# Optimization experiments

Measured on AMD Instinct MI355X. Metric: run time of the kernel, lower is better.

The kernel has to match this reference:

```python
import jax, jax.numpy as jnp
import numpy as np

S, B, T = 16, 32, 64        # max_sents, batch, max_tokens
V, E, H = 50000, 256, 256   # vocab, embed_size, gru_hidden (n_dim)
NC = 50                     # n_classes


def setup_inputs() -> dict:
    key = jax.random.key(0)
    ks = jax.random.split(key, 30)

    def u(k, shape, s=0.1):
        return jax.random.uniform(k, shape, minval=-s, maxval=s, dtype=jnp.float32)

    return {
        "x": jax.random.randint(ks[0], (S, B, T), 0, V, dtype=jnp.int64),
        "embed": jax.random.normal(ks[1], (V, E), dtype=jnp.float32) * 0.1,
        # word-level bi-GRU (input E, hidden H); gate order r,z,n as in torch
        "wg_Wih_f": u(ks[2], (3 * H, E)), "wg_Whh_f": u(ks[3], (3 * H, H)),
        "wg_bih_f": u(ks[4], (3 * H,)),   "wg_bhh_f": u(ks[5], (3 * H,)),
        "wg_Wih_b": u(ks[6], (3 * H, E)), "wg_Whh_b": u(ks[7], (3 * H, H)),
        "wg_bih_b": u(ks[8], (3 * H,)),   "wg_bhh_b": u(ks[9], (3 * H,)),
        "word_W": u(ks[10], (2 * H, 2 * H)),
        "word_b": u(ks[11], (2 * H, 1)),
        "word_proj": u(ks[12], (2 * H, 1)),
        # sentence-level bi-GRU (input 2H, hidden H)
        "sg_Wih_f": u(ks[13], (3 * H, 2 * H)), "sg_Whh_f": u(ks[14], (3 * H, H)),
        "sg_bih_f": u(ks[15], (3 * H,)),       "sg_bhh_f": u(ks[16], (3 * H,)),
        "sg_Wih_b": u(ks[17], (3 * H, 2 * H)), "sg_Whh_b": u(ks[18], (3 * H, H)),
        "sg_bih_b": u(ks[19], (3 * H,)),       "sg_bhh_b": u(ks[20], (3 * H,)),
        "sent_W": u(ks[21], (2 * H, 2 * H)),
        "sent_b": u(ks[22], (2 * H, 1)),
        "sent_proj": u(ks[23], (2 * H, 1)),
        "fin_W": u(ks[24], (NC, 2 * H)),
        "fin_b": u(ks[25], (NC,)),
        "state_word": jnp.zeros((2, B, H), dtype=jnp.float32),
        "state_sent": jnp.zeros((2, B, H), dtype=jnp.float32),
    }


def _gru_dir(x, h0, Wih, Whh, bih, bhh, reverse=False):
    # x: [T, B, in]; returns hidden states [T, B, H] (in original time order)
    xp = jnp.einsum('tbe,ge->tbg', x, Wih) + bih  # precompute input projections

    def step(h, xt):
        g = h @ Whh.T + bhh
        xr, xz, xn = jnp.split(xt, 3, axis=-1)
        hr, hz, hn = jnp.split(g, 3, axis=-1)
        r = jax.nn.sigmoid(xr + hr)
        z = jax.nn.sigmoid(xz + hz)
        n = jnp.tanh(xn + r * hn)
        h = (1.0 - z) * n + z * h
        return h, h

    _, hs = jax.lax.scan(step, h0, xp, reverse=reverse)
    return hs


def _bigru(x, h0, Wf, Hf, bif, bhf, Wb, Hb, bib, bhb):
    f = _gru_dir(x, h0[0], Wf, Hf, bif, bhf, reverse=False)
    b = _gru_dir(x, h0[1], Wb, Hb, bib, bhb, reverse=True)
    return jnp.concatenate([f, b], axis=-1)  # [T, B, 2H]


def _attn_pool(out, W, b, proj):
    # out: [T, B, 2H]; batch_matmul_bias(tanh) -> batch_matmul -> softmax over T -> weighted sum
    squish = jnp.tanh(jnp.einsum('tbh,hk->tbk', out, W) + b[:, 0])  # [T,B,2H]
    scores = jnp.einsum('tbk,k->tb', squish, proj[:, 0])            # [T,B]
    a = jax.nn.softmax(scores, axis=0)                              # softmax over seq
    return jnp.einsum('tb,tbh->bh', a, out)                         # [B,2H]


def reference(x, embed,
              wg_Wih_f, wg_Whh_f, wg_bih_f, wg_bhh_f,
              wg_Wih_b, wg_Whh_b, wg_bih_b, wg_bhh_b,
              word_W, word_b, word_proj,
              sg_Wih_f, sg_Whh_f, sg_bih_f, sg_bhh_f,
              sg_Wih_b, sg_Whh_b, sg_bih_b, sg_bhh_b,
              sent_W, sent_b, sent_proj,
              fin_W, fin_b, state_word, state_sent):
    e = embed[x]                         # [S,B,T,E]
    e = jnp.transpose(e, (0, 2, 1, 3))   # [S,T,B,E] (torch code transposes per sentence)

    word_out = jax.vmap(
        lambda xs: _bigru(xs, state_word,
                          wg_Wih_f, wg_Whh_f, wg_bih_f, wg_bhh_f,
                          wg_Wih_b, wg_Whh_b, wg_bih_b, wg_bhh_b)
    )(e)                                 # [S,T,B,2H]

    s = jax.vmap(lambda o: _attn_pool(o, word_W, word_b, word_proj))(word_out)  # [S,B,2H]

    sent_out = _bigru(s, state_sent,
                      sg_Wih_f, sg_Whh_f, sg_bih_f, sg_bhh_f,
                      sg_Wih_b, sg_Whh_b, sg_bih_b, sg_bhh_b)  # [S,B,2H]
    pooled = _attn_pool(sent_out, sent_W, sent_b, sent_proj)   # [B,2H]
    return pooled @ fin_W.T + fin_b                            # [B,NC] logits
```

## Files before the change

### kernel.cpp

```cpp
#include <hip/hip_runtime.h>


typedef float  f32x4  __attribute__((ext_vector_type(4)));
typedef int    i32x4  __attribute__((ext_vector_type(4)));
typedef __bf16 bf16x8 __attribute__((ext_vector_type(8)));

#define DEVINL static __device__ __forceinline__

DEVINL unsigned short f2bf(float f) {
    unsigned int x = __builtin_bit_cast(unsigned int, f);
    x = x + 0x7fffu + ((x >> 16) & 1u);
    return (unsigned short)(x >> 16);
}
DEVINL float bf2f(unsigned short u) {
    unsigned int x = ((unsigned int)u) << 16;
    return __builtin_bit_cast(float, x);
}
DEVINL float sigm(float x) { return __builtin_amdgcn_rcpf(1.f + __expf(-x)); }
DEVINL float tanh_(float x) {
    x = fminf(fmaxf(x, -20.f), 20.f);
    float e = __expf(-2.f * x);
    return (1.f - e) * __builtin_amdgcn_rcpf(1.f + e);
}
DEVINL void mfma16(f32x4& acc, i32x4 a, i32x4 b) {
    acc = __builtin_amdgcn_mfma_f32_16x16x32_bf16(
        __builtin_bit_cast(bf16x8, a), __builtin_bit_cast(bf16x8, b), acc, 0, 0, 0);
}
DEVINL f32x4 zero4() { f32x4 v = {0.f, 0.f, 0.f, 0.f}; return v; }
DEVINL void gload16(const void* gsrc, void* ldst) {
    __builtin_amdgcn_global_load_lds(
        (const __attribute__((address_space(1))) unsigned int*)gsrc,
        (__attribute__((address_space(3))) unsigned int*)ldst, 16, 0, 0);
}

#define O_WPWF    ((size_t)0)
#define O_WPWB    ((size_t)1048576)
#define O_WPSGIH  ((size_t)2097152)
#define O_WPSHHF  ((size_t)3670016)
#define O_WPSHHB  ((size_t)4063232)
#define O_WPWW    ((size_t)4456448)
#define O_WPSW    ((size_t)4980736)
#define O_BIASWF  ((size_t)5505024)
#define O_BIASWB  ((size_t)5509120)
#define O_BIHCAT  ((size_t)5513216)
#define O_WOUT    ((size_t)5519360)
#define O_SCORESW ((size_t)39073792)
#define O_SSFRAG  ((size_t)39204864)
#define O_XPSENT  ((size_t)39729152)
#define O_SOFRAG  ((size_t)42874880)
#define O_SCORESS ((size_t)43399168)
#define WS_NEED_B ((size_t)43401216)
#define O_EMB16   ((size_t)43401216)
#define O_XPW     ((size_t)69001216)
#define WS_NEED_A ((size_t)169664512)

__global__ void k_prep(const float* wihf, const float* whhf,
                       const float* wihb, const float* whhb,
                       const float* sgihf, const float* sgihb,
                       const float* sghhf, const float* sghhb,
                       const float* wordW, const float* sentW,
                       const float* bihf, const float* bhhf,
                       const float* bihb, const float* bhhb,
                       const float* sgbihf, const float* sgbihb,
                       const float* sgbhhf, const float* sgbhhb,
                       const float* embed,
                       unsigned short* Wpwf, unsigned short* Wpwb,
                       unsigned short* Wpsgih,
                       unsigned short* WpshhF, unsigned short* WpshhB,
                       unsigned short* WpwW, unsigned short* WpsW,
                       float* biasWf, float* biasWb, float* bihCat,
                       unsigned short* emb16, int doEmb)
{
    const int tid0 = blockIdx.x * blockDim.x + threadIdx.x;
    const int nth  = gridDim.x * blockDim.x;

    for (int idx = tid0; idx < 2 * 524288; idx += nth) {
        int d = idx >> 19, sidx = idx & 524287;
        int j = sidx & 7, chunk = sidx >> 3;
        int lane = chunk & 63, nk = chunk >> 6;
        int kf = nk & 15, nf = nk >> 4;
        int n = nf * 16 + (lane & 15);
        int k = kf * 32 + (lane >> 4) * 8 + j;
        const float* Wih = d ? wihb : wihf;
        const float* Whh = d ? whhb : whhf;
        int g4 = n >> 8, jj = n & 255;
        float v = 0.f;
        if (k < 256) {
            if (g4 == 0) v = Wih[jj * 256 + k];
            else if (g4 == 1) v = Wih[(256 + jj) * 256 + k];
            else if (g4 == 2) v = Wih[(512 + jj) * 256 + k];
        } else {
            int kk = k - 256;
            if (g4 == 0) v = Whh[jj * 256 + kk];
            else if (g4 == 1) v = Whh[(256 + jj) * 256 + kk];
            else if (g4 == 3) v = Whh[(512 + jj) * 256 + kk];
        }
        (d ? Wpwb : Wpwf)[sidx] = f2bf(v);
    }
    for (int idx = tid0; idx < 786432; idx += nth) {
        int j = idx & 7, chunk = idx >> 3;
        int lane = chunk & 63, nk = chunk >> 6;
        int kf = nk & 15, nf = nk >> 4;
        int n = nf * 16 + (lane & 15);
        int k = kf * 32 + (lane >> 4) * 8 + j;
        float v = (n < 768) ? sgihf[n * 512 + k] : sgihb[(n - 768) * 512 + k];
        Wpsgih[idx] = f2bf(v);
    }
    for (int idx = tid0; idx < 2 * 196608; idx += nth) {
        int d = idx >= 196608;
        int sidx = d ? idx - 196608 : idx;
        int j = sidx & 7, chunk = sidx >> 3;
        int lane = chunk & 63, nk = chunk >> 6;
        int kf = nk & 7, nf = nk >> 3;
        int n = nf * 16 + (lane & 15);
        int k = kf * 32 + (lane >> 4) * 8 + j;
        float v = (d ? sghhb : sghhf)[n * 256 + k];
        (d ? WpshhB : WpshhF)[sidx] = f2bf(v);
    }
    for (int idx = tid0; idx < 2 * 262144; idx += nth) {
        int d = idx >> 18, sidx = idx & 262143;
        int j = sidx & 7, chunk = sidx >> 3;
        int lane = chunk & 63, nk = chunk >> 6;
        int kf = nk & 15, nf = nk >> 4;
        int n = nf * 16 + (lane & 15);
        int k = kf * 32 + (lane >> 4) * 8 + j;
        float v = (d ? sentW : wordW)[k * 512 + n];
        (d ? WpsW : WpwW)[sidx] = f2bf(v);
    }
    for (int idx = tid0; idx < 2048; idx += nth) {
        int d = idx >> 10, i = idx & 1023;
        int g4 = i >> 8, j = i & 255;
        const float* bi = d ? bihb : bihf;
        const float* bh = d ? bhhb : bhhf;
        float v = (g4 == 0) ? bi[j] + bh[j]
                : (g4 == 1) ? bi[256 + j] + bh[256 + j]
                : (g4 == 2) ? bi[512 + j] : bh[512 + j];
        (d ? biasWb : biasWf)[i] = v;
    }
    for (int idx = tid0; idx < 1536; idx += nth) {
        int d = idx >= 768, j = d ? idx - 768 : idx;
        const float* bi = d ? sgbihb : sgbihf;
        const float* bh = d ? sgbhhb : sgbhhf;
        bihCat[idx] = bi[j] + ((j < 512) ? bh[j] : 0.f);
    }
    if (doEmb) {
        for (int idx = tid0; idx < 3200000; idx += nth) {
            f32x4 v = ((const f32x4*)embed)[idx];
            unsigned int lo = (unsigned)f2bf(v.x) | ((unsigned)f2bf(v.y) << 16);
            unsigned int hi = (unsigned)f2bf(v.z) | ((unsigned)f2bf(v.w) << 16);
            ((unsigned int*)emb16)[idx * 2]     = lo;
            ((unsigned int*)emb16)[idx * 2 + 1] = hi;
        }
    }
}

__global__ __launch_bounds__(512)
void k_xpw(const int* xg, const unsigned short* emb16,
           const unsigned short* Wpwf_u, const unsigned short* Wpwb_u,
           const float* biasWf, const float* biasWb, unsigned short* xpw)
{
    __shared__ unsigned short Abuf[128][256];
    const int tid = threadIdx.x, lane = tid & 63, w = tid >> 6;
    const int cid = blockIdx.x;
    const int tq = cid & 3, bh = (cid >> 2) & 1, dir = (cid >> 3) & 1, s = cid >> 4;
    const int t0 = tq * 16;
    const i32x4* Wp = (const i32x4*)(dir ? Wpwb_u : Wpwf_u);
    const float* biasW = dir ? biasWb : biasWf;

    i32x4 B[3][2][8];
#pragma unroll
    for (int g = 0; g < 3; ++g)
#pragma unroll
        for (int q = 0; q < 2; ++q)
#pragma unroll
            for (int kk = 0; kk < 8; ++kk)
                B[g][q][kk] = Wp[((g * 16 + w * 2 + q) * 16 + kk) * 64 + lane];

    float bias_rg[3][2];
#pragma unroll
    for (int g = 0; g < 3; ++g)
#pragma unroll
        for (int q = 0; q < 2; ++q)
            bias_rg[g][q] = biasW[g * 256 + (w * 2 + q) * 16 + (lane & 15)];

    for (int ch = 0; ch < 2; ++ch) {
        __syncthreads();
#pragma unroll
        for (int c = 0; c < 8; ++c) {
            const int trow = 16 * w + 2 * c + (lane >> 5);
            const int b = trow & 15;
            const int tok = xg[(s * 32 + bh * 16 + b) * 64 + (t0 + ch * 8 + w)];
            const int kbyte = ((lane & 31) * 16) ^ ((trow & 7) << 4);
            gload16((const char*)emb16 + (size_t)tok * 512 + kbyte,
                    (char*)&Abuf[0][0] + (w * 8 + c) * 1024);
        }
        __syncthreads();

#pragma unroll 1
        for (int tl = 0; tl < 8; ++tl) {
            f32x4 acc[3][2];
#pragma unroll
            for (int g = 0; g < 3; ++g) { acc[g][0] = zero4(); acc[g][1] = zero4(); }
#pragma unroll
            for (int kk = 0; kk < 8; ++kk) {
                const int row = tl * 16 + (lane & 15);
                const int boff = (kk * 64 + (lane >> 4) * 16) ^ ((row & 7) << 4);
                i32x4 a = *(const i32x4*)((const char*)&Abuf[row][0] + boff);
#pragma unroll
                for (int g = 0; g < 3; ++g) {
                    mfma16(acc[g][0], a, B[g][0][kk]);
                    mfma16(acc[g][1], a, B[g][1][kk]);
                }
            }
            const int t = t0 + ch * 8 + tl;
            const int tb = (((s * 2 + dir) * 2 + bh) * 64 + t) * 12288;
#pragma unroll
            for (int g = 0; g < 3; ++g)
#pragma unroll
                for (int q = 0; q < 2; ++q) {
                    const int j = (w * 2 + q) * 16 + (lane & 15);
                    const float bb = bias_rg[g][q];
                    unsigned int lo = (unsigned)f2bf(acc[g][q][0] + bb) |
                                      ((unsigned)f2bf(acc[g][q][1] + bb) << 16);
                    unsigned int hi = (unsigned)f2bf(acc[g][q][2] + bb) |
                                      ((unsigned)f2bf(acc[g][q][3] + bb) << 16);
                    uint2 pk; pk.x = lo; pk.y = hi;
                    *(uint2*)(xpw + tb + (g * 256 + j) * 16 + 4 * (lane >> 4)) = pk;
                }
        }
    }
}

__global__ __launch_bounds__(512)
void k_gru_wordA(const float* stateW,
                 const unsigned short* Wpwf_u, const unsigned short* Wpwb_u,
                 const float* biasWf, const float* biasWb,
                 const unsigned short* xpw, unsigned short* wout)
{
    __shared__ unsigned short Abuf[2][16][256];
    __shared__ unsigned short xpL[2][12288];
    const int tid = threadIdx.x, lane = tid & 63, w = tid >> 6;
    const int cid = blockIdx.x;
    const int bh = cid & 1, dir = (cid >> 1) & 1, s = cid >> 2;
    const i32x4* Wp = (const i32x4*)(dir ? Wpwb_u : Wpwf_u);
    const float* biasW = dir ? biasWb : biasWf;
    const int gmap[3] = {0, 1, 3};

    i32x4 B[3][2][8];
#pragma unroll
    for (int g = 0; g < 3; ++g)
#pragma unroll
        for (int q = 0; q < 2; ++q)
#pragma unroll
            for (int kk = 0; kk < 8; ++kk)
                B[g][q][kk] = Wp[((gmap[g] * 16 + w * 2 + q) * 16 + 8 + kk) * 64 + lane];

    float bhn[2];
    float hreg[2][4];
#pragma unroll
    for (int q = 0; q < 2; ++q) {
        const int j = (w * 2 + q) * 16 + (lane & 15);
        bhn[q] = biasW[768 + j];
#pragma unroll
        for (int i = 0; i < 4; ++i) {
            const int b = 4 * (lane >> 4) + i;
            float h0 = stateW[dir * 8192 + (bh * 16 + b) * 256 + j];
            hreg[q][i] = h0;
            int byteoff = b * 512 + ((j * 2) ^ ((b & 7) << 4));
            *(unsigned short*)((char*)&Abuf[0][0][0] + byteoff) = f2bf(h0);
        }
    }
    const size_t xbase = (size_t)(((s * 2 + dir) * 2 + bh) * 64) * 24576;
    const int tfirst = dir ? 63 : 0;
#pragma unroll
    for (int c = 0; c < 3; ++c)
        gload16((const char*)xpw + xbase + (size_t)tfirst * 24576 +
                    ((w * 3 + c) * 64 + lane) * 16,
                (char*)&xpL[0][0] + (w * 3 + c) * 1024);

    for (int ti = 0; ti < 64; ++ti) {
        __syncthreads();
        const int t = dir ? 63 - ti : ti;
        const int cur = ti & 1, nxt = cur ^ 1;
        if (ti < 63) {
            const int tn = dir ? t - 1 : t + 1;
#pragma unroll
            for (int c = 0; c < 3; ++c)
                gload16((const char*)xpw + xbase + (size_t)tn * 24576 +
                            ((w * 3 + c) * 64 + lane) * 16,
                        (char*)&xpL[nxt][0] + (w * 3 + c) * 1024);
        }
        f32x4 acc[3][2];
#pragma unroll
        for (int g = 0; g < 3; ++g) { acc[g][0] = zero4(); acc[g][1] = zero4(); }
#pragma unroll
        for (int kk = 0; kk < 8; ++kk) {
            const int row = lane & 15;
            const int boff = (kk * 64 + (lane >> 4) * 16) ^ ((row & 7) << 4);
            i32x4 a = *(const i32x4*)((const char*)&Abuf[cur][row][0] + boff);
#pragma unroll
            for (int g = 0; g < 3; ++g) {
                mfma16(acc[g][0], a, B[g][0][kk]);
                mfma16(acc[g][1], a, B[g][1][kk]);
            }
        }
#pragma unroll
        for (int q = 0; q < 2; ++q) {
            const int j = (w * 2 + q) * 16 + (lane & 15);
            uint2 xr = *(const uint2*)((const char*)&xpL[cur][0] +
                        ((0 * 256 + j) * 16 + 4 * (lane >> 4)) * 2);
            uint2 xz = *(const uint2*)((const char*)&xpL[cur][0] +
                        ((1 * 256 + j) * 16 + 4 * (lane >> 4)) * 2);
            uint2 xn = *(const uint2*)((const char*)&xpL[cur][0] +
                        ((2 * 256 + j) * 16 + 4 * (lane >> 4)) * 2);
            float xrf[4] = { bf2f((unsigned short)(xr.x & 0xffffu)),
                             bf2f((unsigned short)(xr.x >> 16)),
                             bf2f((unsigned short)(xr.y & 0xffffu)),
                             bf2f((unsigned short)(xr.y >> 16)) };
            float xzf[4] = { bf2f((unsigned short)(xz.x & 0xffffu)),
                             bf2f((unsigned short)(xz.x >> 16)),
                             bf2f((unsigned short)(xz.y & 0xffffu)),
                             bf2f((unsigned short)(xz.y >> 16)) };
            float xnf[4] = { bf2f((unsigned short)(xn.x & 0xffffu)),
                             bf2f((unsigned short)(xn.x >> 16)),
                             bf2f((unsigned short)(xn.y & 0xffffu)),
                             bf2f((unsigned short)(xn.y >> 16)) };
#pragma unroll
            for (int i = 0; i < 4; ++i) {
                const int b = 4 * (lane >> 4) + i;
                float rv = sigm(xrf[i] + acc[0][q][i]);
                float zv = sigm(xzf[i] + acc[1][q][i]);
                float nv = tanh_(xnf[i] + rv * (acc[2][q][i] + bhn[q]));
                float hnew = (1.f - zv) * nv + zv * hreg[q][i];
                hreg[q][i] = hnew;
                unsigned short hb = f2bf(hnew);
                int byteoff = b * 512 + ((j * 2) ^ ((b & 7) << 4));
                *(unsigned short*)((char*)&Abuf[nxt][0][0] + byteoff) = hb;
                const int r = (s * 64 + t) * 32 + bh * 16 + b;
                const int hcol = dir * 256 + j;
                wout[(((r >> 4) * 16 + (hcol >> 5)) * 64 + (r & 15) +
                      ((hcol >> 3) & 3) * 16) * 8 + (hcol & 7)] = hb;
            }
        }
    }
}

DEVINL void prefetchE(unsigned short (*Ab)[512], const int* xg, const float* embed,
                      int s, int t, int tid)
{
    const int brow = tid >> 5, c = tid & 31;
    const int tok = xg[(s * 32 + brow) * 64 + t];
    const f32x4* src = (const f32x4*)(embed + (size_t)tok * 256) + c * 2;
    f32x4 f0 = src[0], f1 = src[1];
    i32x4 pk;
    pk.x = (int)((unsigned)f2bf(f0.x) | ((unsigned)f2bf(f0.y) << 16));
    pk.y = (int)((unsigned)f2bf(f0.z) | ((unsigned)f2bf(f0.w) << 16));
    pk.z = (int)((unsigned)f2bf(f1.x) | ((unsigned)f2bf(f1.y) << 16));
    pk.w = (int)((unsigned)f2bf(f1.z) | ((unsigned)f2bf(f1.w) << 16));
    int kbyte = (c * 16) ^ ((brow & 7) << 4);
    *(i32x4*)((char*)&Ab[brow][0] + kbyte) = pk;
}

__global__ __launch_bounds__(1024, 4)
void k_gru_word(const int* xg, const float* embed, const float* stateW,
                const unsigned short* Wpwf_u, const unsigned short* Wpwb_u,
                const float* biasWf, const float* biasWb,
                unsigned short* wout)
{
    __shared__ unsigned short Abuf[2][32][512];

    const int tid = threadIdx.x, lane = tid & 63, w = tid >> 6;
    const int cid = blockIdx.x, s = cid >> 1, dir = cid & 1;
    const i32x4* Wp = (const i32x4*)(dir ? Wpwb_u : Wpwf_u);
    const float* bias = dir ? biasWb : biasWf;

    const int j = w * 16 + (lane & 15);
    float hreg[2][4];
#pragma unroll
    for (int mf = 0; mf < 2; ++mf)
#pragma unroll
        for (int i = 0; i < 4; ++i) {
            int b = mf * 16 + (lane >> 4) * 4 + i;
            float h0 = stateW[dir * 8192 + b * 256 + j];
            hreg[mf][i] = h0;
            int byteoff = ((256 + j) * 2) ^ ((b & 7) << 4);
            *(unsigned short*)((char*)&Abuf[0][b][0] + byteoff) = f2bf(h0);
        }
    const int tfirst = dir ? 63 : 0;
    prefetchE(Abuf[0], xg, embed, s, tfirst, tid);

    const float br = bias[j], bz = bias[256 + j];
    const float bxn = bias[512 + j], bhn = bias[768 + j];

    for (int ti = 0; ti < 64; ++ti) {
        __syncthreads();
        const int t = dir ? 63 - ti : ti;
        const int cur = ti & 1, nxt = cur ^ 1;
        if (ti < 63) prefetchE(Abuf[nxt], xg, embed, s, dir ? t - 1 : t + 1, tid);

        f32x4 acc[4][2];
#pragma unroll
        for (int g = 0; g < 4; ++g) { acc[g][0] = zero4(); acc[g][1] = zero4(); }

        i32x4 bbuf[3][3];
#define LOADB_W(KF, DST)                                                     \
        {                                                                    \
            const int gX = ((KF) < 8) ? 32 : 48;                             \
            DST[0] = Wp[((0 + w)  * 16 + (KF)) * 64 + lane];                 \
            DST[1] = Wp[((16 + w) * 16 + (KF)) * 64 + lane];                 \
            DST[2] = Wp[((gX + w) * 16 + (KF)) * 64 + lane];                 \
        }
        LOADB_W(0, bbuf[0]);
        LOADB_W(1, bbuf[1]);

#pragma unroll
        for (int kf = 0; kf < 16; ++kf) {
            if (kf < 14) LOADB_W(kf + 2, bbuf[(kf + 2) % 3]);
            const int row0 = lane & 15;
            const int boff = (kf * 64 + (lane >> 4) * 16) ^ ((row0 & 7) << 4);
            i32x4 a0 = *(const i32x4*)((const char*)&Abuf[cur][row0][0] + boff);
            i32x4 a1 = *(const i32x4*)((const char*)&Abuf[cur][16 + row0][0] + boff);
            const i32x4* bc = bbuf[kf % 3];
            mfma16(acc[0][0], a0, bc[0]); mfma16(acc[0][1], a1, bc[0]);
            mfma16(acc[1][0], a0, bc[1]); mfma16(acc[1][1], a1, bc[1]);
            if (kf < 8) { mfma16(acc[2][0], a0, bc[2]);
                          mfma16(acc[2][1], a1, bc[2]); }
            else        { mfma16(acc[3][0], a0, bc[2]);
                          mfma16(acc[3][1], a1, bc[2]); }
        }
#undef LOADB_W

#pragma unroll
        for (int mf = 0; mf < 2; ++mf)
#pragma unroll
            for (int i = 0; i < 4; ++i) {
                const int b = mf * 16 + (lane >> 4) * 4 + i;
                float rv = sigm(acc[0][mf][i] + br);
                float zv = sigm(acc[1][mf][i] + bz);
                float nv = tanh_(acc[2][mf][i] + bxn +
                                 rv * (acc[3][mf][i] + bhn));
                float hnew = (1.f - zv) * nv + zv * hreg[mf][i];
                hreg[mf][i] = hnew;
                unsigned short hb = f2bf(hnew);
                int byteoff = ((256 + j) * 2) ^ ((b & 7) << 4);
                *(unsigned short*)((char*)&Abuf[nxt][b][0] + byteoff) = hb;
                int r = (s * 64 + t) * 32 + b;
                int hcol = dir * 256 + j;
                wout[(((r >> 4) * 16 + (hcol >> 5)) * 64 + (r & 15) +
                      ((hcol >> 3) & 3) * 16) * 8 + (hcol & 7)] = hb;
            }
    }
}

__global__ __launch_bounds__(512, 4)
void k_attn_score2(const unsigned short* Afrag_u, const unsigned short* Wp_u,
                   const float* wb, const float* wp, float* scores)
{
    __shared__ i32x4 Wl[2][16][64];
    const int tid = threadIdx.x, lane = tid & 63, w = tid >> 6;
    const int rblk = blockIdx.x * 8 + w;
    const i32x4* A = (const i32x4*)Afrag_u;
    const i32x4* Wg = (const i32x4*)Wp_u;

    i32x4 a[16];
#pragma unroll
    for (int kf = 0; kf < 16; ++kf) a[kf] = A[(rblk * 16 + kf) * 64 + lane];

    i32x4* wl0 = &Wl[0][0][0];
    i32x4* wl1 = &Wl[1][0][0];
    wl0[tid] = Wg[tid]; wl0[tid + 512] = Wg[tid + 512];

    float partial[4] = {};
    for (int nf = 0; nf < 32; ++nf) {
        __syncthreads();
        if (nf < 31) {
            i32x4* dst = (nf & 1) ? wl0 : wl1;
            dst[tid]       = Wg[(nf + 1) * 1024 + tid];
            dst[tid + 512] = Wg[(nf + 1) * 1024 + tid + 512];
        }
        const i32x4* cur = (nf & 1) ? wl1 : wl0;
        f32x4 acc0 = zero4(), acc1 = zero4();
#pragma unroll
        for (int kf = 0; kf < 16; kf += 2) {
            mfma16(acc0, a[kf],     cur[kf * 64 + lane]);
            mfma16(acc1, a[kf + 1], cur[(kf + 1) * 64 + lane]);
        }
        const int n = nf * 16 + (lane & 15);
        const float wbn = wb[n], wpn = wp[n];
#pragma unroll
        for (int i = 0; i < 4; ++i)
            partial[i] += tanh_(acc0[i] + acc1[i] + wbn) * wpn;
    }
#pragma unroll
    for (int i = 0; i < 4; ++i) {
        float v = partial[i];
        v += __shfl_xor(v, 1); v += __shfl_xor(v, 2);
        v += __shfl_xor(v, 4); v += __shfl_xor(v, 8);
        if ((lane & 15) == 0)
            scores[rblk * 16 + (lane >> 4) * 4 + i] = v;
    }
}

__global__ void k_attn_score_small(const unsigned short* Afrag_u,
                                   const unsigned short* Wp_u,
                                   const float* wb, const float* wp, float* scores)
{
    const int tid = threadIdx.x, lane = tid & 63, w = tid >> 6;
    const int rblk = blockIdx.x * 4 + w;
    const i32x4* A = (const i32x4*)Afrag_u;
    const i32x4* Wp = (const i32x4*)Wp_u;
    i32x4 a[16];
#pragma unroll
    for (int kf = 0; kf < 16; ++kf) a[kf] = A[(rblk * 16 + kf) * 64 + lane];

    float partial[4] = {};
    for (int nf = 0; nf < 32; ++nf) {
        f32x4 acc0 = zero4(), acc1 = zero4();
#pragma unroll
        for (int kf = 0; kf < 16; kf += 2) {
            mfma16(acc0, a[kf],     Wp[(nf * 16 + kf) * 64 + lane]);
            mfma16(acc1, a[kf + 1], Wp[(nf * 16 + kf + 1) * 64 + lane]);
        }
        const int n = nf * 16 + (lane & 15);
        const float wbn = wb[n], wpn = wp[n];
#pragma unroll
        for (int i = 0; i < 4; ++i)
            partial[i] += tanh_(acc0[i] + acc1[i] + wbn) * wpn;
    }
#pragma unroll
    for (int i = 0; i < 4; ++i) {
        float v = partial[i];
        v += __shfl_xor(v, 1); v += __shfl_xor(v, 2);
        v += __shfl_xor(v, 4); v += __shfl_xor(v, 8);
        if ((lane & 15) == 0)
            scores[rblk * 16 + (lane >> 4) * 4 + i] = v;
    }
}

__global__ void k_word_pool(const float* scores, const unsigned short* wout,
                            unsigned short* ssFrag)
{
    __shared__ float aL[64];
    const int l = threadIdx.x;
    const int bid = blockIdx.x;
    const int s = bid >> 5, b = bid & 31;
    float sc = scores[s * 2048 + l * 32 + b];
    float m = sc;
#pragma unroll
    for (int d = 1; d < 64; d <<= 1) m = fmaxf(m, __shfl_xor(m, d));
    float e = __expf(sc - m), sum = e;
#pragma unroll
    for (int d = 1; d < 64; d <<= 1) sum += __shfl_xor(sum, d);
    aL[l] = e * __builtin_amdgcn_rcpf(sum);
    __syncthreads();

    float acc[8] = {};
    const i32x4* WO = (const i32x4*)wout;
    for (int t = 0; t < 64; ++t) {
        float at = aL[t];
        int cidx = ((s * 128 + t * 2 + (b >> 4)) * 16 + (l >> 2)) * 64 +
                   (b & 15) + (l & 3) * 16;
        i32x4 ch = WO[cidx];
        acc[0] += at * bf2f((unsigned short)((unsigned)ch.x & 0xffffu));
        acc[1] += at * bf2f((unsigned short)((unsigned)ch.x >> 16));
        acc[2] += at * bf2f((unsigned short)((unsigned)ch.y & 0xffffu));
        acc[3] += at * bf2f((unsigned short)((unsigned)ch.y >> 16));
        acc[4] += at * bf2f((unsigned short)((unsigned)ch.z & 0xffffu));
        acc[5] += at * bf2f((unsigned short)((unsigned)ch.z >> 16));
        acc[6] += at * bf2f((unsigned short)((unsigned)ch.w & 0xffffu));
        acc[7] += at * bf2f((unsigned short)((unsigned)ch.w >> 16));
    }
    i32x4 pk;
    pk.x = (int)((unsigned)f2bf(acc[0]) | ((unsigned)f2bf(acc[1]) << 16));
    pk.y = (int)((unsigned)f2bf(acc[2]) | ((unsigned)f2bf(acc[3]) << 16));
    pk.z = (int)((unsigned)f2bf(acc[4]) | ((unsigned)f2bf(acc[5]) << 16));
    pk.w = (int)((unsigned)f2bf(acc[6]) | ((unsigned)f2bf(acc[7]) << 16));
    const int r2 = s * 32 + b;
    int cidx2 = ((r2 >> 4) * 16 + (l >> 2)) * 64 + (r2 & 15) + (l & 3) * 16;
    ((i32x4*)ssFrag)[cidx2] = pk;
}

__global__ void k_sgih(const unsigned short* ssFrag_u, const unsigned short* Wp_u,
                       const float* bihCat, float* xpSent)
{
    const int tid = threadIdx.x, lane = tid & 63, w = tid >> 6;
    const int rblk = blockIdx.x, ncl = blockIdx.y;
    const i32x4* A = (const i32x4*)ssFrag_u;
    const i32x4* Wp = (const i32x4*)Wp_u;
    i32x4 a[16];
#pragma unroll
    for (int kf = 0; kf < 16; ++kf) a[kf] = A[(rblk * 16 + kf) * 64 + lane];
#pragma unroll
    for (int nfl = 0; nfl < 4; ++nfl) {
        const int nfg = ncl * 16 + w * 4 + nfl;
        f32x4 acc = zero4();
#pragma unroll
        for (int kf = 0; kf < 16; ++kf)
            mfma16(acc, a[kf], Wp[(nfg * 16 + kf) * 64 + lane]);
        const int n = nfg * 16 + (lane & 15);
        const float bb = bihCat[n];
        const int dir = n >= 768, ng = n - dir * 768;
        const int g = ng >> 8, jj = ng & 255;
#pragma unroll
        for (int i = 0; i < 4; ++i) {
            int row = rblk * 16 + (lane >> 4) * 4 + i;
            int s = row >> 5, b = row & 31;
            xpSent[(((dir * 2 + (b >> 4)) * 16 + s) * 12288) +
                   (g * 256 + jj) * 16 + (b & 15)] = acc[i] + bb;
        }
    }
}

__global__ __launch_bounds__(512)
void k_gru_sentA(const float* stateS, const unsigned short* WpF_u,
                 const unsigned short* WpB_u, const float* bhhf, const float* bhhb,
                 const float* xpSent, unsigned short* soFrag)
{
    __shared__ unsigned short Abuf[2][16][256];
    __shared__ float xpLs[2][12288];
    const int tid = threadIdx.x, lane = tid & 63, w = tid >> 6;
    const int cid = blockIdx.x, bh = cid & 1, dir = cid >> 1;
    const i32x4* Wp = (const i32x4*)(dir ? WpB_u : WpF_u);
    const float* bhh = dir ? bhhb : bhhf;

    i32x4 B[3][2][8];
#pragma unroll
    for (int g = 0; g < 3; ++g)
#pragma unroll
        for (int q = 0; q < 2; ++q)
#pragma unroll
            for (int kk = 0; kk < 8; ++kk)
                B[g][q][kk] = Wp[((g * 16 + w * 2 + q) * 8 + kk) * 64 + lane];

    float bhn[2];
    float hreg[2][4];
#pragma unroll
    for (int q = 0; q < 2; ++q) {
        const int j = (w * 2 + q) * 16 + (lane & 15);
        bhn[q] = bhh[512 + j];
#pragma unroll
        for (int i = 0; i < 4; ++i) {
            const int b = 4 * (lane >> 4) + i;
            float h0 = stateS[dir * 8192 + (bh * 16 + b) * 256 + j];
            hreg[q][i] = h0;
            int byteoff = b * 512 + ((j * 2) ^ ((b & 7) << 4));
            *(unsigned short*)((char*)&Abuf[0][0][0] + byteoff) = f2bf(h0);
        }
    }
    const size_t xbase = (size_t)((dir * 2 + bh) * 16) * 49152;
    const int sfirst = dir ? 15 : 0;
#pragma unroll
    for (int c = 0; c < 6; ++c)
        gload16((const char*)xpSent + xbase + (size_t)sfirst * 49152 +
                    ((w * 6 + c) * 64 + lane) * 16,
                (char*)&xpLs[0][0] + (w * 6 + c) * 1024);

    for (int si = 0; si < 16; ++si) {
        __syncthreads();
        const int s = dir ? 15 - si : si;
        const int cur = si & 1, nxt = cur ^ 1;
        if (si < 15) {
            const int sn = dir ? s - 1 : s + 1;
#pragma unroll
// ... 106 lines not shown
extern "C" void kernel_launch(void* const* d_in, const int* in_sizes, int n_in,
                              void* d_out, int out_size, void* d_ws, size_t ws_size,
                              hipStream_t stream)
{
    if (ws_size < WS_NEED_B) return;
    const int bigA = (ws_size >= WS_NEED_A) ? 1 : 0;

    const int*   x      = (const int*)d_in[0];
    const float* embed  = (const float*)d_in[1];
    const float* wgWihF = (const float*)d_in[2];
    const float* wgWhhF = (const float*)d_in[3];
    const float* wgBihF = (const float*)d_in[4];
    const float* wgBhhF = (const float*)d_in[5];
    const float* wgWihB = (const float*)d_in[6];
    const float* wgWhhB = (const float*)d_in[7];
    const float* wgBihB = (const float*)d_in[8];
    const float* wgBhhB = (const float*)d_in[9];
    const float* wordW  = (const float*)d_in[10];
    const float* wordB  = (const float*)d_in[11];
    const float* wordP  = (const float*)d_in[12];
    const float* sgWihF = (const float*)d_in[13];
    const float* sgWhhF = (const float*)d_in[14];
    const float* sgBihF = (const float*)d_in[15];
    const float* sgBhhF = (const float*)d_in[16];
    const float* sgWihB = (const float*)d_in[17];
    const float* sgWhhB = (const float*)d_in[18];
    const float* sgBihB = (const float*)d_in[19];
    const float* sgBhhB = (const float*)d_in[20];
    const float* sentWm = (const float*)d_in[21];
    const float* sentB  = (const float*)d_in[22];
    const float* sentP  = (const float*)d_in[23];
    const float* finW   = (const float*)d_in[24];
    const float* finB   = (const float*)d_in[25];
    const float* stateW = (const float*)d_in[26];
    const float* stateS = (const float*)d_in[27];

    char* ws = (char*)d_ws;
    unsigned short* Wpwf   = (unsigned short*)(ws + O_WPWF);
    unsigned short* Wpwb   = (unsigned short*)(ws + O_WPWB);
    unsigned short* Wpsgih = (unsigned short*)(ws + O_WPSGIH);
    unsigned short* WpshhF = (unsigned short*)(ws + O_WPSHHF);
    unsigned short* WpshhB = (unsigned short*)(ws + O_WPSHHB);
    unsigned short* WpwW   = (unsigned short*)(ws + O_WPWW);
    unsigned short* WpsW   = (unsigned short*)(ws + O_WPSW);
    float* biasWf  = (float*)(ws + O_BIASWF);
    float* biasWb  = (float*)(ws + O_BIASWB);
    float* bihCat  = (float*)(ws + O_BIHCAT);
    unsigned short* wout   = (unsigned short*)(ws + O_WOUT);
    float* scoresW = (float*)(ws + O_SCORESW);
    unsigned short* ssFrag = (unsigned short*)(ws + O_SSFRAG);
    float* xpSent  = (float*)(ws + O_XPSENT);
    unsigned short* soFrag = (unsigned short*)(ws + O_SOFRAG);
    float* scoresS = (float*)(ws + O_SCORESS);
    unsigned short* emb16  = (unsigned short*)(ws + O_EMB16);
    unsigned short* xpw    = (unsigned short*)(ws + O_XPW);

    k_prep<<<512, 256, 0, stream>>>(wgWihF, wgWhhF, wgWihB, wgWhhB,
                                    sgWihF, sgWihB, sgWhhF, sgWhhB,
                                    wordW, sentWm,
                                    wgBihF, wgBhhF, wgBihB, wgBhhB,
                                    sgBihF, sgBihB, sgBhhF, sgBhhB, embed,
                                    Wpwf, Wpwb, Wpsgih, WpshhF, WpshhB,
                                    WpwW, WpsW, biasWf, biasWb, bihCat,
                                    emb16, bigA);

    if (bigA) {
        k_xpw<<<256, 512, 0, stream>>>(x, emb16, Wpwf, Wpwb, biasWf, biasWb, xpw);
        k_gru_wordA<<<64, 512, 0, stream>>>(stateW, Wpwf, Wpwb, biasWf, biasWb,
                                            xpw, wout);
    } else {
        k_gru_word<<<32, 1024, 0, stream>>>(x, embed, stateW, Wpwf, Wpwb,
                                            biasWf, biasWb, wout);
    }

    k_attn_score2<<<256, 512, 0, stream>>>(wout, WpwW, wordB, wordP, scoresW);
    k_word_pool<<<512, 64, 0, stream>>>(scoresW, wout, ssFrag);

    k_sgih<<<dim3(32, 6), 256, 0, stream>>>(ssFrag, Wpsgih, bihCat, xpSent);
    k_gru_sentA<<<4, 512, 0, stream>>>(stateS, WpshhF, WpshhB, sgBhhF, sgBhhB,
                                       xpSent, soFrag);

    k_attn_score_small<<<8, 256, 0, stream>>>(soFrag, WpsW, sentB, sentP, scoresS);
    k_sent_pool_fin<<<32, 256, 0, stream>>>(scoresS, soFrag, finW, finB,
                                            (float*)d_out);
}
```

Before: 449.4 us.

## Drop full-vocab bf16 embedding conversion and restructure word GRU pipelines

```diff
diff --git a/kernel.cpp b/kernel.cpp
--- a/kernel.cpp
+++ b/kernel.cpp
@@ -15,6 +15,9 @@
 DEVINL float bf2f(unsigned short u) {
     unsigned int x = ((unsigned int)u) << 16;
     return __builtin_bit_cast(float, x);
+}
+DEVINL float bfe16(unsigned int v, int hi) {
+    return bf2f((unsigned short)(hi ? (v >> 16) : (v & 0xffffu)));
 }
 DEVINL float sigm(float x) { return __builtin_amdgcn_rcpf(1.f + __expf(-x)); }
 DEVINL float tanh_(float x) {
@@ -27,11 +30,6 @@
         __builtin_bit_cast(bf16x8, a), __builtin_bit_cast(bf16x8, b), acc, 0, 0, 0);
 }
 DEVINL f32x4 zero4() { f32x4 v = {0.f, 0.f, 0.f, 0.f}; return v; }
-DEVINL void gload16(const void* gsrc, void* ldst) {
-    __builtin_amdgcn_global_load_lds(
-        (const __attribute__((address_space(1))) unsigned int*)gsrc,
-        (__attribute__((address_space(3))) unsigned int*)ldst, 16, 0, 0);
-}
 
 #define O_WPWF    ((size_t)0)
 #define O_WPWB    ((size_t)1048576)
@@ -50,9 +48,8 @@
 #define O_SOFRAG  ((size_t)42874880)
 #define O_SCORESS ((size_t)43399168)
 #define WS_NEED_B ((size_t)43401216)
-#define O_EMB16   ((size_t)43401216)
-#define O_XPW     ((size_t)69001216)
-#define WS_NEED_A ((size_t)169664512)
+#define O_XPW     ((size_t)43401216)
+#define WS_NEED_A ((size_t)144064512)
 
 __global__ void k_prep(const float* wihf, const float* whhf,
                        const float* wihb, const float* whhb,
@@ -63,13 +60,11 @@
                        const float* bihb, const float* bhhb,
                        const float* sgbihf, const float* sgbihb,
                        const float* sgbhhf, const float* sgbhhb,
-                       const float* embed,
                        unsigned short* Wpwf, unsigned short* Wpwb,
                        unsigned short* Wpsgih,
                        unsigned short* WpshhF, unsigned short* WpshhB,
                        unsigned short* WpwW, unsigned short* WpsW,
-                       float* biasWf, float* biasWb, float* bihCat,
-                       unsigned short* emb16, int doEmb)
+                       float* biasWf, float* biasWb, float* bihCat)
 {
     const int tid0 = blockIdx.x * blockDim.x + threadIdx.x;
     const int nth  = gridDim.x * blockDim.x;
@@ -143,204 +138,194 @@
         const float* bh = d ? sgbhhb : sgbhhf;
         bihCat[idx] = bi[j] + ((j < 512) ? bh[j] : 0.f);
     }
-    if (doEmb) {
-        for (int idx = tid0; idx < 3200000; idx += nth) {
-            f32x4 v = ((const f32x4*)embed)[idx];
-            unsigned int lo = (unsigned)f2bf(v.x) | ((unsigned)f2bf(v.y) << 16);
-            unsigned int hi = (unsigned)f2bf(v.z) | ((unsigned)f2bf(v.w) << 16);
-            ((unsigned int*)emb16)[idx * 2]     = lo;
-            ((unsigned int*)emb16)[idx * 2 + 1] = hi;
-        }
-    }
-}
-
-__global__ __launch_bounds__(512)
-void k_xpw(const int* xg, const unsigned short* emb16,
+}
+
+__global__ __launch_bounds__(512, 2)
+void k_xpw(const int* xg, const float* embed,
            const unsigned short* Wpwf_u, const unsigned short* Wpwb_u,
            const float* biasWf, const float* biasWb, unsigned short* xpw)
 {
-    __shared__ unsigned short Abuf[128][256];
+    __shared__ unsigned short Ebuf[2][16][256];
     const int tid = threadIdx.x, lane = tid & 63, w = tid >> 6;
     const int cid = blockIdx.x;
     const int tq = cid & 3, bh = (cid >> 2) & 1, dir = (cid >> 3) & 1, s = cid >> 4;
     const int t0 = tq * 16;
     const i32x4* Wp = (const i32x4*)(dir ? Wpwb_u : Wpwf_u);
     const float* biasW = dir ? biasWb : biasWf;
-
-    i32x4 B[3][2][8];
+    const int b = lane & 15, rsub = lane >> 4;
+
+    i32x4 A[3][2][8];
 #pragma unroll
     for (int g = 0; g < 3; ++g)
 #pragma unroll
         for (int q = 0; q < 2; ++q)
 #pragma unroll
             for (int kk = 0; kk < 8; ++kk)
-                B[g][q][kk] = Wp[((g * 16 + w * 2 + q) * 16 + kk) * 64 + lane];
-
-    float bias_rg[3][2];
+                A[g][q][kk] = Wp[((g * 16 + w * 2 + q) * 16 + kk) * 64 + lane];
+
+    unsigned int biasp[3][2][2];
 #pragma unroll
     for (int g = 0; g < 3; ++g)
 #pragma unroll
-        for (int q = 0; q < 2; ++q)
-            bias_rg[g][q] = biasW[g * 256 + (w * 2 + q) * 16 + (lane & 15)];
-
-    for (int ch = 0; ch < 2; ++ch) {
+        for (int q = 0; q < 2; ++q) {
+            const int j0 = g * 256 + (w * 2 + q) * 16 + rsub * 4;
+            biasp[g][q][0] = (unsigned)f2bf(biasW[j0]) |
+                             ((unsigned)f2bf(biasW[j0 + 1]) << 16);
+            biasp[g][q][1] = (unsigned)f2bf(biasW[j0 + 2]) |
+                             ((unsigned)f2bf(biasW[j0 + 3]) << 16);
+        }
+
+    const int sb = tid >> 5, sc = tid & 31;
+    const int tokrow = (s * 32 + bh * 16 + sb) * 64;
+    const int sdst = sb * 512 + ((sc * 16) ^ ((sb & 7) << 4));
+
+#define STAGE_E(BUF, T)                                                       \
+    {                                                                         \
+        const int tok = xg[tokrow + (T)];                                     \
+        const f32x4* src = (const f32x4*)(embed + (size_t)tok * 256 + sc * 8);\
+        f32x4 e0 = src[0], e1 = src[1];                                       \
+        i32x4 pk;                                                             \
+        pk.x = (int)((unsigned)f2bf(e0.x) | ((unsigned)f2bf(e0.y) << 16));    \
+        pk.y = (int)((unsigned)f2bf(e0.z) | ((unsigned)f2bf(e0.w) << 16));    \
+        pk.z = (int)((unsigned)f2bf(e1.x) | ((unsigned)f2bf(e1.y) << 16));    \
+        pk.w = (int)((unsigned)f2bf(e1.z) | ((unsigned)f2bf(e1.w) << 16));    \
+        *(i32x4*)((char*)&Ebuf[BUF][0][0] + sdst) = pk;                       \
+    }
+
+    STAGE_E(0, t0);
+    const size_t chain = (size_t)((s * 2 + dir) * 2 + bh);
+    char* const xpBase = (char*)xpw + chain * 1572864 +
+                         (size_t)(rsub * 128 + b * 8);
+
+    for (int tl = 0; tl < 16; ++tl) {
         __syncthreads();
-#pragma unroll
-        for (int c = 0; c < 8; ++c) {
-            const int trow = 16 * w + 2 * c + (lane >> 5);
-            const int b = trow & 15;
-            const int tok = xg[(s * 32 + bh * 16 + b) * 64 + (t0 + ch * 8 + w)];
-            const int kbyte = ((lane & 31) * 16) ^ ((trow & 7) << 4);
-            gload16((const char*)emb16 + (size_t)tok * 512 + kbyte,
-                    (char*)&Abuf[0][0] + (w * 8 + c) * 1024);
-        }
-        __syncthreads();
-
-#pragma unroll 1
-        for (int tl = 0; tl < 8; ++tl) {
-            f32x4 acc[3][2];
-#pragma unroll
-            for (int g = 0; g < 3; ++g) { acc[g][0] = zero4(); acc[g][1] = zero4(); }
-#pragma unroll
-            for (int kk = 0; kk < 8; ++kk) {
-                const int row = tl * 16 + (lane & 15);
-                const int boff = (kk * 64 + (lane >> 4) * 16) ^ ((row & 7) << 4);
-                i32x4 a = *(const i32x4*)((const char*)&Abuf[row][0] + boff);
-#pragma unroll
-                for (int g = 0; g < 3; ++g) {
-                    mfma16(acc[g][0], a, B[g][0][kk]);
-                    mfma16(acc[g][1], a, B[g][1][kk]);
-                }
+        const int t = t0 + tl, cur = tl & 1, nxt = cur ^ 1;
+        if (tl < 15) STAGE_E(nxt, t + 1);
+
+        f32x4 acc[3][2];
+#pragma unroll
+        for (int g = 0; g < 3; ++g) { acc[g][0] = zero4(); acc[g][1] = zero4(); }
+#pragma unroll
+        for (int kk = 0; kk < 8; ++kk) {
+            const int roff = b * 512 + ((kk * 64 + rsub * 16) ^ ((b & 7) << 4));
+            i32x4 eb = *(const i32x4*)((const char*)&Ebuf[cur][0][0] + roff);
+            mfma16(acc[0][0], A[0][0][kk], eb); mfma16(acc[0][1], A[0][1][kk], eb);
+            mfma16(acc[1][0], A[1][0][kk], eb); mfma16(acc[1][1], A[1][1][kk], eb);
+            mfma16(acc[2][0], A[2][0][kk], eb); mfma16(acc[2][1], A[2][1][kk], eb);
+        }
+        char* ob = xpBase + (size_t)t * 24576;
+#pragma unroll
+        for (int g = 0; g < 3; ++g)
+#pragma unroll
+            for (int q = 0; q < 2; ++q) {
+                unsigned short us[4];
+#pragma unroll
+                for (int i = 0; i < 4; ++i)
+                    us[i] = f2bf(acc[g][q][i] + bfe16(biasp[g][q][i >> 1], i & 1));
+                uint2 pk;
+                pk.x = (unsigned)us[0] | ((unsigned)us[1] << 16);
+                pk.y = (unsigned)us[2] | ((unsigned)us[3] << 16);
+                *(uint2*)(ob + g * 8192 + (w * 2 + q) * 512) = pk;
             }
-            const int t = t0 + ch * 8 + tl;
-            const int tb = (((s * 2 + dir) * 2 + bh) * 64 + t) * 12288;
-#pragma unroll
-            for (int g = 0; g < 3; ++g)
-#pragma unroll
-                for (int q = 0; q < 2; ++q) {
-                    const int j = (w * 2 + q) * 16 + (lane & 15);
-                    const float bb = bias_rg[g][q];
-                    unsigned int lo = (unsigned)f2bf(acc[g][q][0] + bb) |
-                                      ((unsigned)f2bf(acc[g][q][1] + bb) << 16);
-                    unsigned int hi = (unsigned)f2bf(acc[g][q][2] + bb) |
-                                      ((unsigned)f2bf(acc[g][q][3] + bb) << 16);
-                    uint2 pk; pk.x = lo; pk.y = hi;
-                    *(uint2*)(xpw + tb + (g * 256 + j) * 16 + 4 * (lane >> 4)) = pk;
-                }
-        }
-    }
-}
-
-__global__ __launch_bounds__(512)
+    }
+#undef STAGE_E
+}
+
+__global__ __launch_bounds__(512, 2)
 void k_gru_wordA(const float* stateW,
                  const unsigned short* Wpwf_u, const unsigned short* Wpwb_u,
                  const float* biasWf, const float* biasWb,
                  const unsigned short* xpw, unsigned short* wout)
 {
-    __shared__ unsigned short Abuf[2][16][256];
-    __shared__ unsigned short xpL[2][12288];
+    __shared__ unsigned short Hbuf[2][16][256];
     const int tid = threadIdx.x, lane = tid & 63, w = tid >> 6;
-    const int cid = blockIdx.x;
-    const int bh = cid & 1, dir = (cid >> 1) & 1, s = cid >> 2;
+    const int cid = blockIdx.x, bh = cid & 1, dir = (cid >> 1) & 1, s = cid >> 2;
     const i32x4* Wp = (const i32x4*)(dir ? Wpwb_u : Wpwf_u);
     const float* biasW = dir ? biasWb : biasWf;
+    const int b = lane & 15, rsub = lane >> 4;
     const int gmap[3] = {0, 1, 3};
 
-    i32x4 B[3][2][8];
+    i32x4 A[3][2][8];
 #pragma unroll
     for (int g = 0; g < 3; ++g)
 #pragma unroll
         for (int q = 0; q < 2; ++q)
 #pragma unroll
             for (int kk = 0; kk < 8; ++kk)
-                B[g][q][kk] = Wp[((gmap[g] * 16 + w * 2 + q) * 16 + 8 + kk) * 64 + lane];
-
-    float bhn[2];
+                A[g][q][kk] =
+                    Wp[((gmap[g] * 16 + w * 2 + q) * 16 + 8 + kk) * 64 + lane];
+
+    unsigned int bhnp[2][2];
     float hreg[2][4];
 #pragma unroll
     for (int q = 0; q < 2; ++q) {
-        const int j = (w * 2 + q) * 16 + (lane & 15);
-        bhn[q] = biasW[768 + j];
-#pragma unroll
-        for (int i = 0; i < 4; ++i) {
-            const int b = 4 * (lane >> 4) + i;
-            float h0 = stateW[dir * 8192 + (bh * 16 + b) * 256 + j];
-            hreg[q][i] = h0;
-            int byteoff = b * 512 + ((j * 2) ^ ((b & 7) << 4));
-            *(unsigned short*)((char*)&Abuf[0][0][0] + byteoff) = f2bf(h0);
-        }
-    }
-    const size_t xbase = (size_t)(((s * 2 + dir) * 2 + bh) * 64) * 24576;
-    const int tfirst = dir ? 63 : 0;
-#pragma unroll
-    for (int c = 0; c < 3; ++c)
-        gload16((const char*)xpw + xbase + (size_t)tfirst * 24576 +
-                    ((w * 3 + c) * 64 + lane) * 16,
-                (char*)&xpL[0][0] + (w * 3 + c) * 1024);
+        const int j0 = (w * 2 + q) * 16 + rsub * 4;
+        f32x4 h0 = *(const f32x4*)(stateW + dir * 8192 + (bh * 16 + b) * 256 + j0);
+        bhnp[q][0] = (unsigned)f2bf(biasW[768 + j0]) |
+                     ((unsigned)f2bf(biasW[768 + j0 + 1]) << 16);
+        bhnp[q][1] = (unsigned)f2bf(biasW[768 + j0 + 2]) |
+                     ((unsigned)f2bf(biasW[768 + j0 + 3]) << 16);
+        hreg[q][0] = h0.x; hreg[q][1] = h0.y; hreg[q][2] = h0.z; hreg[q][3] = h0.w;
+        uint2 pk;
+        pk.x = (unsigned)f2bf(h0.x) | ((unsigned)f2bf(h0.y) << 16);
+        pk.y = (unsigned)f2bf(h0.z) | ((unsigned)f2bf(h0.w) << 16);
+        const int boff = b * 512 + (((w * 2 + q) * 32 + rsub * 8) ^ ((b & 7) << 4));
+        *(uint2*)((char*)&Hbuf[0][0][0] + boff) = pk;
+    }
+    const size_t chain = (size_t)((s * 2 + dir) * 2 + bh);
+    const char* const xpBase = (const char*)xpw + chain * 1572864 +
+                               (size_t)(rsub * 128 + b * 8);
 
     for (int ti = 0; ti < 64; ++ti) {
         __syncthreads();
         const int t = dir ? 63 - ti : ti;
         const int cur = ti & 1, nxt = cur ^ 1;
-        if (ti < 63) {
-            const int tn = dir ? t - 1 : t + 1;
-#pragma unroll
-            for (int c = 0; c < 3; ++c)
-                gload16((const char*)xpw + xbase + (size_t)tn * 24576 +
-                            ((w * 3 + c) * 64 + lane) * 16,
-                        (char*)&xpL[nxt][0] + (w * 3 + c) * 1024);
-        }
+
+        uint2 xpv[3][2];
+        const char* xb = xpBase + (size_t)t * 24576;
+#pragma unroll
+        for (int g = 0; g < 3; ++g)
+#pragma unroll
+            for (int q = 0; q < 2; ++q)
+                xpv[g][q] = *(const uint2*)(xb + g * 8192 + (w * 2 + q) * 512);
+
         f32x4 acc[3][2];
 #pragma unroll
         for (int g = 0; g < 3; ++g) { acc[g][0] = zero4(); acc[g][1] = zero4(); }
 #pragma unroll
         for (int kk = 0; kk < 8; ++kk) {
-            const int row = lane & 15;
-            const int boff = (kk * 64 + (lane >> 4) * 16) ^ ((row & 7) << 4);
-            i32x4 a = *(const i32x4*)((const char*)&Abuf[cur][row][0] + boff);
-#pragma unroll
-            for (int g = 0; g < 3; ++g) {
-                mfma16(acc[g][0], a, B[g][0][kk]);
-                mfma16(acc[g][1], a, B[g][1][kk]);
+            const int roff = b * 512 + ((kk * 64 + rsub * 16) ^ ((b & 7) << 4));
+            i32x4 hb = *(const i32x4*)((const char*)&Hbuf[cur][0][0] + roff);
+            mfma16(acc[0][0], A[0][0][kk], hb); mfma16(acc[0][1], A[0][1][kk], hb);
+            mfma16(acc[1][0], A[1][0][kk], hb); mfma16(acc[1][1], A[1][1][kk], hb);
+            mfma16(acc[2][0], A[2][0][kk], hb); mfma16(acc[2][1], A[2][1][kk], hb);
+        }
+        const int r = (s * 64 + t) * 32 + bh * 16 + b;
+#pragma unroll
+        for (int q = 0; q < 2; ++q) {
+            unsigned short us[4];
+#pragma unroll
+            for (int i = 0; i < 4; ++i) {
+                const unsigned xr = (i < 2) ? xpv[0][q].x : xpv[0][q].y;
+                const unsigned xz = (i < 2) ? xpv[1][q].x : xpv[1][q].y;
+                const unsigned xn = (i < 2) ? xpv[2][q].x : xpv[2][q].y;
+                float rv = sigm(bfe16(xr, i & 1) + acc[0][q][i]);
+                float zv = sigm(bfe16(xz, i & 1) + acc[1][q][i]);
+                float nv = tanh_(bfe16(xn, i & 1) +
+                                 rv * (acc[2][q][i] + bfe16(bhnp[q][i >> 1], i & 1)));
+                float h = (1.f - zv) * nv + zv * hreg[q][i];
+                hreg[q][i] = h;
+                us[i] = f2bf(h);
             }
-        }
-#pragma unroll
-        for (int q = 0; q < 2; ++q) {
-            const int j = (w * 2 + q) * 16 + (lane & 15);
-            uint2 xr = *(const uint2*)((const char*)&xpL[cur][0] +
-                        ((0 * 256 + j) * 16 + 4 * (lane >> 4)) * 2);
-            uint2 xz = *(const uint2*)((const char*)&xpL[cur][0] +
-                        ((1 * 256 + j) * 16 + 4 * (lane >> 4)) * 2);
-            uint2 xn = *(const uint2*)((const char*)&xpL[cur][0] +
-                        ((2 * 256 + j) * 16 + 4 * (lane >> 4)) * 2);
-            float xrf[4] = { bf2f((unsigned short)(xr.x & 0xffffu)),
-                             bf2f((unsigned short)(xr.x >> 16)),
-                             bf2f((unsigned short)(xr.y & 0xffffu)),
-                             bf2f((unsigned short)(xr.y >> 16)) };
-            float xzf[4] = { bf2f((unsigned short)(xz.x & 0xffffu)),
-                             bf2f((unsigned short)(xz.x >> 16)),
-                             bf2f((unsigned short)(xz.y & 0xffffu)),
-                             bf2f((unsigned short)(xz.y >> 16)) };
-            float xnf[4] = { bf2f((unsigned short)(xn.x & 0xffffu)),
-                             bf2f((unsigned short)(xn.x >> 16)),
-                             bf2f((unsigned short)(xn.y & 0xffffu)),
-                             bf2f((unsigned short)(xn.y >> 16)) };
-#pragma unroll
-            for (int i = 0; i < 4; ++i) {
-                const int b = 4 * (lane >> 4) + i;
-                float rv = sigm(xrf[i] + acc[0][q][i]);
-                float zv = sigm(xzf[i] + acc[1][q][i]);
-                float nv = tanh_(xnf[i] + rv * (acc[2][q][i] + bhn[q]));
-                float hnew = (1.f - zv) * nv + zv * hreg[q][i];
-                hreg[q][i] = hnew;
-                unsigned short hb = f2bf(hnew);
-                int byteoff = b * 512 + ((j * 2) ^ ((b & 7) << 4));
-                *(unsigned short*)((char*)&Abuf[nxt][0][0] + byteoff) = hb;
-                const int r = (s * 64 + t) * 32 + bh * 16 + b;
-                const int hcol = dir * 256 + j;
-                wout[(((r >> 4) * 16 + (hcol >> 5)) * 64 + (r & 15) +
-                      ((hcol >> 3) & 3) * 16) * 8 + (hcol & 7)] = hb;
-            }
+            uint2 pk;
+            pk.x = (unsigned)us[0] | ((unsigned)us[1] << 16);
+            pk.y = (unsigned)us[2] | ((unsigned)us[3] << 16);
+            const int boff = b * 512 + (((w * 2 + q) * 32 + rsub * 8) ^ ((b & 7) << 4));
+            *(uint2*)((char*)&Hbuf[nxt][0][0] + boff) = pk;
+            const int hcol = dir * 256 + (w * 2 + q) * 16 + rsub * 4;
+            const int widx = (((r >> 4) * 16 + (hcol >> 5)) * 64 + (r & 15) +
+                              ((hcol >> 3) & 3) * 16) * 8 + (hcol & 7);
+            *(uint2*)(wout + widx) = pk;
         }
     }
 }
@@ -368,7 +353,6 @@
                 unsigned short* wout)
 {
     __shared__ unsigned short Abuf[2][32][512];
-
     const int tid = threadIdx.x, lane = tid & 63, w = tid >> 6;
     const int cid = blockIdx.x, s = cid >> 1, dir = cid & 1;
     const i32x4* Wp = (const i32x4*)(dir ? Wpwb_u : Wpwf_u);
@@ -412,7 +396,6 @@
         }
         LOADB_W(0, bbuf[0]);
         LOADB_W(1, bbuf[1]);
-
 #pragma unroll
         for (int kf = 0; kf < 16; ++kf) {
             if (kf < 14) LOADB_W(kf + 2, bbuf[(kf + 2) % 3]);
@@ -429,7 +412,6 @@
                           mfma16(acc[3][1], a1, bc[2]); }
         }
 #undef LOADB_W
-
 #pragma unroll
         for (int mf = 0; mf < 2; ++mf)
 #pragma unroll
@@ -437,8 +419,7 @@
                 const int b = mf * 16 + (lane >> 4) * 4 + i;
                 float rv = sigm(acc[0][mf][i] + br);
                 float zv = sigm(acc[1][mf][i] + bz);
-                float nv = tanh_(acc[2][mf][i] + bxn +
-                                 rv * (acc[3][mf][i] + bhn));
+                float nv = tanh_(acc[2][mf][i] + bxn + rv * (acc[3][mf][i] + bhn));
                 float hnew = (1.f - zv) * nv + zv * hreg[mf][i];
                 hreg[mf][i] = hnew;
                 unsigned short hb = f2bf(hnew);
@@ -452,13 +433,13 @@
     }
 }
 
-__global__ __launch_bounds__(512, 4)
+__global__ __launch_bounds__(1024, 4)
 void k_attn_score2(const unsigned short* Afrag_u, const unsigned short* Wp_u,
                    const float* wb, const float* wp, float* scores)
 {
     __shared__ i32x4 Wl[2][16][64];
     const int tid = threadIdx.x, lane = tid & 63, w = tid >> 6;
-    const int rblk = blockIdx.x * 8 + w;
+    const int rblk = blockIdx.x * 16 + w;
     const i32x4* A = (const i32x4*)Afrag_u;
     const i32x4* Wg = (const i32x4*)Wp_u;
 
@@ -468,15 +449,14 @@
 
     i32x4* wl0 = &Wl[0][0][0];
     i32x4* wl1 = &Wl[1][0][0];
-    wl0[tid] = Wg[tid]; wl0[tid + 512] = Wg[tid + 512];
+    wl0[tid] = Wg[tid];
 
     float partial[4] = {};
     for (int nf = 0; nf < 32; ++nf) {
         __syncthreads();
         if (nf < 31) {
             i32x4* dst = (nf & 1) ? wl0 : wl1;
-            dst[tid]       = Wg[(nf + 1) * 1024 + tid];
-            dst[tid + 512] = Wg[(nf + 1) * 1024 + tid + 512];
+            dst[tid] = Wg[(nf + 1) * 1024 + tid];
         }
         const i32x4* cur = (nf & 1) ? wl1 : wl0;
         f32x4 acc0 = zero4(), acc1 = zero4();
@@ -541,22 +521,26 @@
                             unsigned short* ssFrag)
 {
     __shared__ float aL[64];
-    const int l = threadIdx.x;
+    __shared__ float part[4][64][8];
+    const int tid = threadIdx.x, l = tid & 63, w = tid >> 6;
     const int bid = blockIdx.x;
     const int s = bid >> 5, b = bid & 31;
-    float sc = scores[s * 2048 + l * 32 + b];
-    float m = sc;
-#pragma unroll
-    for (int d = 1; d < 64; d <<= 1) m = fmaxf(m, __shfl_xor(m, d));
-    float e = __expf(sc - m), sum = e;
-#pragma unroll
-    for (int d = 1; d < 64; d <<= 1) sum += __shfl_xor(sum, d);
-    aL[l] = e * __builtin_amdgcn_rcpf(sum);
+    if (w == 0) {
+        float sc = scores[s * 2048 + l * 32 + b];
+        float m = sc;
+#pragma unroll
+        for (int d = 1; d < 64; d <<= 1) m = fmaxf(m, __shfl_xor(m, d));
+        float e = __expf(sc - m), sum = e;
+#pragma unroll
+        for (int d = 1; d < 64; d <<= 1) sum += __shfl_xor(sum, d);
+        aL[l] = e * __builtin_amdgcn_rcpf(sum);
+    }
     __syncthreads();
 
     float acc[8] = {};
     const i32x4* WO = (const i32x4*)wout;
-    for (int t = 0; t < 64; ++t) {
+    for (int tt = 0; tt < 16; ++tt) {
+        const int t = w * 16 + tt;
         float at = aL[t];
         int cidx = ((s * 128 + t * 2 + (b >> 4)) * 16 + (l >> 2)) * 64 +
                    (b & 15) + (l & 3) * 16;
@@ -570,14 +554,23 @@
         acc[6] += at * bf2f((unsigned short)((unsigned)ch.w & 0xffffu));
         acc[7] += at * bf2f((unsigned short)((unsigned)ch.w >> 16));
     }
-    i32x4 pk;
-    pk.x = (int)((unsigned)f2bf(acc[0]) | ((unsigned)f2bf(acc[1]) << 16));
-    pk.y = (int)((unsigned)f2bf(acc[2]) | ((unsigned)f2bf(acc[3]) << 16));
-    pk.z = (int)((unsigned)f2bf(acc[4]) | ((unsigned)f2bf(acc[5]) << 16));
-    pk.w = (int)((unsigned)f2bf(acc[6]) | ((unsigned)f2bf(acc[7]) << 16));
-    const int r2 = s * 32 + b;
-    int cidx2 = ((r2 >> 4) * 16 + (l >> 2)) * 64 + (r2 & 15) + (l & 3) * 16;
-    ((i32x4*)ssFrag)[cidx2] = pk;
+#pragma unroll
+    for (int q = 0; q < 8; ++q) part[w][l][q] = acc[q];
+    __syncthreads();
+    if (w == 0) {
+        float fin[8];
+#pragma unroll
+        for (int q = 0; q < 8; ++q)
+            fin[q] = part[0][l][q] + part[1][l][q] + part[2][l][q] + part[3][l][q];
+        i32x4 pk;
+        pk.x = (int)((unsigned)f2bf(fin[0]) | ((unsigned)f2bf(fin[1]) << 16));
+        pk.y = (int)((unsigned)f2bf(fin[2]) | ((unsigned)f2bf(fin[3]) << 16));
+        pk.z = (int)((unsigned)f2bf(fin[4]) | ((unsigned)f2bf(fin[5]) << 16));
+        pk.w = (int)((unsigned)f2bf(fin[6]) | ((unsigned)f2bf(fin[7]) << 16));
+        const int r2 = s * 32 + b;
+        int cidx2 = ((r2 >> 4) * 16 + (l >> 2)) * 64 + (r2 & 15) + (l & 3) * 16;
+        ((i32x4*)ssFrag)[cidx2] = pk;
+    }
 }
 
 __global__ void k_sgih(const unsigned short* ssFrag_u, const unsigned short* Wp_u,
@@ -609,6 +602,12 @@
                    (g * 256 + jj) * 16 + (b & 15)] = acc[i] + bb;
         }
     }
+}
+
+DEVINL void gload16(const void* gsrc, void* ldst) {
+    __builtin_amdgcn_global_load_lds(
+        (const __attribute__((address_space(1))) unsigned int*)gsrc,
+        (__attribute__((address_space(3))) unsigned int*)ldst, 16, 0, 0);
 }
 
 __global__ __launch_bounds__(512)
@@ -821,20 +820,18 @@
     float* xpSent  = (float*)(ws + O_XPSENT);
     unsigned short* soFrag = (unsigned short*)(ws + O_SOFRAG);
     float* scoresS = (float*)(ws + O_SCORESS);
-    unsigned short* emb16  = (unsigned short*)(ws + O_EMB16);
     unsigned short* xpw    = (unsigned short*)(ws + O_XPW);
 
     k_prep<<<512, 256, 0, stream>>>(wgWihF, wgWhhF, wgWihB, wgWhhB,
                                     sgWihF, sgWihB, sgWhhF, sgWhhB,
                                     wordW, sentWm,
                                     wgBihF, wgBhhF, wgBihB, wgBhhB,
-                                    sgBihF, sgBihB, sgBhhF, sgBhhB, embed,
+                                    sgBihF, sgBihB, sgBhhF, sgBhhB,
                                     Wpwf, Wpwb, Wpsgih, WpshhF, WpshhB,
-                                    WpwW, WpsW, biasWf, biasWb, bihCat,
-                                    emb16, bigA);
+                                    WpwW, WpsW, biasWf, biasWb, bihCat);
 
     if (bigA) {
-        k_xpw<<<256, 512, 0, stream>>>(x, emb16, Wpwf, Wpwb, biasWf, biasWb, xpw);
+        k_xpw<<<256, 512, 0, stream>>>(x, embed, Wpwf, Wpwb, biasWf, biasWb, xpw);
         k_gru_wordA<<<64, 512, 0, stream>>>(stateW, Wpwf, Wpwb, biasWf, biasWb,
                                             xpw, wout);
     } else {
@@ -842,8 +839,8 @@
                                             biasWf, biasWb, wout);
     }
 
-    k_attn_score2<<<256, 512, 0, stream>>>(wout, WpwW, wordB, wordP, scoresW);
-    k_word_pool<<<512, 64, 0, stream>>>(scoresW, wout, ssFrag);
+    k_attn_score2<<<128, 1024, 0, stream>>>(wout, WpwW, wordB, wordP, scoresW);
+    k_word_pool<<<512, 256, 0, stream>>>(scoresW, wout, ssFrag);
 
     k_sgih<<<dim3(32, 6), 256, 0, stream>>>(ssFrag, Wpsgih, bihCat, xpSent);
     k_gru_sentA<<<4, 512, 0, stream>>>(stateS, WpshhF, WpshhB, sgBhhF, sgBhhB,
```

Measured after the change: 445.2 us. Within noise of the previous version (-0.9%).
